# Kernel optimization log

Hardware: AMD Instinct MI355X
Metric: run time of the kernel (lower is better)

The kernel has to match this reference:

```python
import jax, jax.numpy as jnp
import numpy as np

NUM_HEADS = 16
D_MODEL = 1024
NEG_INF = -1e30


def setup_inputs() -> dict:
    key = jax.random.key(0)
    ks = jax.random.split(key, 7)
    B, S, D = 2, 2048, D_MODEL
    scale = 1.0 / np.sqrt(D)
    return {
        "queries": jax.random.normal(ks[0], (B, S, D), dtype=jnp.float32),
        "keys": jax.random.normal(ks[1], (B, S, D), dtype=jnp.float32),
        "values": jax.random.normal(ks[2], (B, S, D), dtype=jnp.float32),
        "Wq": jax.random.normal(ks[3], (D, D), dtype=jnp.float32) * scale,
        "Wk": jax.random.normal(ks[4], (D, D), dtype=jnp.float32) * scale,
        "Wv": jax.random.normal(ks[5], (D, D), dtype=jnp.float32) * scale,
        "Wo": jax.random.normal(ks[6], (D, D), dtype=jnp.float32) * scale,
    }


def _split_heads(x, h):
    # [B, S, D] -> [B, h, S, D/h]
    B, S, D = x.shape
    return x.reshape(B, S, h, D // h).transpose(0, 2, 1, 3)


def reference(queries, keys, values, Wq, Wk, Wv, Wo):
    h = NUM_HEADS
    q = _split_heads(queries @ Wq, h)  # [B, h, S, dh]
    k = _split_heads(keys @ Wk, h)
    v = _split_heads(values @ Wv, h)
    dh = q.shape[-1]
    scores = jnp.einsum("bhqd,bhkd->bhqk", q, k) / jnp.sqrt(jnp.float32(dh))
    # original quirk: exactly-zero scores are masked to -1e30 before softmax
    scores = jnp.where(scores == 0, NEG_INF, scores)
    attn = jax.nn.softmax(scores, axis=-1)
    out = jnp.einsum("bhqk,bhkd->bhqd", attn, v)  # [B, h, S, dh]
    B, _, S, _ = out.shape
    out = out.transpose(0, 2, 1, 3).reshape(B, S, h * dh)
    return out @ Wo
```

## Files before the change

kernel.cpp:

```cpp
#include <hip/hip_runtime.h>

typedef unsigned short u16;
typedef short bf16x8 __attribute__((ext_vector_type(8)));
typedef float f32x4 __attribute__((ext_vector_type(4)));
typedef float f32x16 __attribute__((ext_vector_type(16)));

namespace {

constexpr int kB = 2, kS = 2048, kD = 1024, kH = 16, kDh = 64;
constexpr float kC2 = 0.125f * 1.44269504088896341f;

__device__ inline u16 f32_bf16(float f) {
    unsigned u = __float_as_uint(f);
    u += 0x7FFFu + ((u >> 16) & 1u);
    return (u16)(u >> 16);
}

__device__ inline u16 f32_bf16_fast(float f) {
    return (u16)((__float_as_uint(f) + 0x8000u) >> 16);
}

__device__ inline float fast_exp2(float x) {
    float r;
    asm("v_exp_f32 %0, %1" : "=v"(r) : "v"(x));
    return r;
}

__device__ inline void gl_lds16(const void* g, void* l) {
    __builtin_amdgcn_global_load_lds(
        (const __attribute__((address_space(1))) void*)g,
        (__attribute__((address_space(3))) void*)l, 16, 0, 0);
}

__device__ inline int swz8(int l) {
    return ((l & 3) ^ ((l >> 2) & 3) ^ ((l >> 4) & 3)) * 8;
}

__global__ __launch_bounds__(256) void prep(
    const float* __restrict__ s0, const float* __restrict__ s1,
    const float* __restrict__ s2,
    u16* __restrict__ d0, u16* __restrict__ d1, u16* __restrict__ d2,
    const float* __restrict__ W0, const float* __restrict__ W1,
    const float* __restrict__ W2, const float* __restrict__ W3,
    u16* __restrict__ T0, u16* __restrict__ T1,
    u16* __restrict__ T2, u16* __restrict__ T3)
{
    const int y = blockIdx.y;
    if (y < 3) {
        const float* src = y == 0 ? s0 : (y == 1 ? s1 : s2);
        u16* dst = y == 0 ? d0 : (y == 1 ? d1 : d2);
        const int i = blockIdx.x * 256 + threadIdx.x;
        const float4* s4 = (const float4*)src;
        float4 a = s4[2 * i], b = s4[2 * i + 1];
        uint4 o;
        o.x = (unsigned)f32_bf16(a.x) | ((unsigned)f32_bf16(a.y) << 16);
        o.y = (unsigned)f32_bf16(a.z) | ((unsigned)f32_bf16(a.w) << 16);
        o.z = (unsigned)f32_bf16(b.x) | ((unsigned)f32_bf16(b.y) << 16);
        o.w = (unsigned)f32_bf16(b.z) | ((unsigned)f32_bf16(b.w) << 16);
        ((uint4*)dst)[i] = o;
        return;
    }
    if (blockIdx.x >= 256) return;
    const int z = y - 3;
    const float* W = z == 0 ? W0 : (z == 1 ? W1 : (z == 2 ? W2 : W3));
    u16* Wt = z == 0 ? T0 : (z == 1 ? T1 : (z == 2 ? T2 : T3));
    const float sc = (z == 0) ? kC2 : 1.0f;

    __shared__ __attribute__((aligned(16))) u16 T[64][65];
    const int t = threadIdx.x;
    const int n0 = (blockIdx.x & 15) * 64, k0 = (blockIdx.x >> 4) * 64;
    const int r = t >> 4, c4 = (t & 15) * 4;
#pragma unroll
    for (int it = 0; it < 4; ++it) {
        const int rr = r + 16 * it;
        float4 v = *(const float4*)(W + (size_t)(k0 + rr) * kD + n0 + c4);
        T[rr][c4 + 0] = f32_bf16(v.x * sc);
        T[rr][c4 + 1] = f32_bf16(v.y * sc);
        T[rr][c4 + 2] = f32_bf16(v.z * sc);
        T[rr][c4 + 3] = f32_bf16(v.w * sc);
    }
    __syncthreads();
#pragma unroll
    for (int it = 0; it < 4; ++it) {
        const int nn = r + 16 * it;
        uint2 pk;
        pk.x = (unsigned)T[c4 + 0][nn] | ((unsigned)T[c4 + 1][nn] << 16);
        pk.y = (unsigned)T[c4 + 2][nn] | ((unsigned)T[c4 + 3][nn] << 16);
        *(uint2*)(Wt + (size_t)(n0 + nn) * kD + k0 + c4) = pk;
    }
}

__global__ __launch_bounds__(256) void vtrans(
    const u16* __restrict__ V, u16* __restrict__ Vt)
{
    __shared__ __attribute__((aligned(16))) u16 T[64][65];
    const int t = threadIdx.x;
    const int s0 = blockIdx.x * 64;
    const int bh = blockIdx.y, b = bh >> 4, h = bh & 15;
    const int rr = t >> 3, c0 = (t & 7) * 8;
    union { u16 u[8]; uint4 v4; } buf;
#pragma unroll
    for (int p = 0; p < 2; ++p) {
        const int s = rr + 32 * p;
        buf.v4 = *(const uint4*)(V + (size_t)(b * kS + s0 + s) * kD + h * kDh + c0);
#pragma unroll
        for (int i = 0; i < 8; ++i) T[c0 + i][s] = buf.u[i];
    }
    __syncthreads();
#pragma unroll
    for (int p = 0; p < 2; ++p) {
        const int d = rr + 32 * p;
#pragma unroll
        for (int i = 0; i < 8; ++i) buf.u[i] = T[d][c0 + i];
        *(uint4*)(Vt + (size_t)(bh * kDh + d) * kS + s0 + c0) = buf.v4;
    }
}

template <bool F32OUT>
__device__ inline void gemm128_body(
    const u16* __restrict__ A, const u16* __restrict__ Wt,
    void* __restrict__ Cout, int M, int N, int K, int bx, int by)
{
    __shared__ __attribute__((aligned(16))) u16 As[128 * 32];
    __shared__ __attribute__((aligned(16))) u16 Bs[128 * 32];
    const int t = threadIdx.x, w = t >> 6, l = t & 63;
    const int quad = l >> 4, c = l & 15;
    const int wm = w >> 1, wn = w & 1;
    const int m0 = by * 128, n0 = bx * 128;
    const int lr = l >> 2, lc = swz8(l);
    const int xc = ((quad ^ (c & 3) ^ ((c >> 2) & 3))) * 8;

    const u16* ga0 = A  + (size_t)(m0 + w * 32 + lr) * K + lc;
    const u16* ga1 = A  + (size_t)(m0 + w * 32 + 16 + lr) * K + lc;
    const u16* gb0 = Wt + (size_t)(n0 + w * 32 + lr) * K + lc;
    const u16* gb1 = Wt + (size_t)(n0 + w * 32 + 16 + lr) * K + lc;
    u16* la0 = &As[(w * 32) * 32];
    u16* la1 = &As[(w * 32 + 16) * 32];
    u16* lb0 = &Bs[(w * 32) * 32];
    u16* lb1 = &Bs[(w * 32 + 16) * 32];

    f32x4 acc[4][4];
#pragma unroll
    for (int mi = 0; mi < 4; ++mi)
#pragma unroll
        for (int nj = 0; nj < 4; ++nj) acc[mi][nj] = 0;

    for (int k0 = 0; k0 < K; k0 += 32) {
        gl_lds16(ga0 + k0, la0);
        gl_lds16(ga1 + k0, la1);
        gl_lds16(gb0 + k0, lb0);
        gl_lds16(gb1 + k0, lb1);
        __syncthreads();
        bf16x8 af[4], bf[4];
#pragma unroll
        for (int mi = 0; mi < 4; ++mi)
            af[mi] = *(const bf16x8*)&As[(wm * 64 + mi * 16 + c) * 32 + xc];
#pragma unroll
        for (int nj = 0; nj < 4; ++nj)
            bf[nj] = *(const bf16x8*)&Bs[(wn * 64 + nj * 16 + c) * 32 + xc];
#pragma unroll
        for (int mi = 0; mi < 4; ++mi)
#pragma unroll
            for (int nj = 0; nj < 4; ++nj)
                acc[mi][nj] = __builtin_amdgcn_mfma_f32_16x16x32_bf16(
                    af[mi], bf[nj], acc[mi][nj], 0, 0, 0);
        __syncthreads();
    }

#pragma unroll
    for (int mi = 0; mi < 4; ++mi)
#pragma unroll
        for (int nj = 0; nj < 4; ++nj)
#pragma unroll
            for (int r = 0; r < 4; ++r) {
                const size_t row = m0 + wm * 64 + mi * 16 + quad * 4 + r;
                const size_t col = n0 + wn * 64 + nj * 16 + c;
                if (F32OUT)
                    ((float*)Cout)[row * N + col] = acc[mi][nj][r];
                else
                    ((u16*)Cout)[row * N + col] = f32_bf16(acc[mi][nj][r]);
            }
}

__global__ __launch_bounds__(256) void gemm_qkv(
    const u16* __restrict__ A0, const u16* __restrict__ A1,
    const u16* __restrict__ A2,
    const u16* __restrict__ W0, const u16* __restrict__ W1,
    const u16* __restrict__ W2,
    u16* __restrict__ C0, u16* __restrict__ C1, u16* __restrict__ C2)
{
    const int z = blockIdx.z;
    const u16* A  = z == 0 ? A0 : (z == 1 ? A1 : A2);
    const u16* Wt = z == 0 ? W0 : (z == 1 ? W1 : W2);
    u16* C = z == 0 ? C0 : (z == 1 ? C1 : C2);
    gemm128_body<false>(A, Wt, C, kB * kS, kD, kD, blockIdx.x, blockIdx.y);
}

__global__ __launch_bounds__(256) void gemm_out(
    const u16* __restrict__ A, const u16* __restrict__ Wt,
    float* __restrict__ C)
{
    __shared__ __attribute__((aligned(16))) u16 As[64 * 32];
    __shared__ __attribute__((aligned(16))) u16 Bs[128 * 32];
    const int N = kD, K = kD;
    const int t = threadIdx.x, w = t >> 6, l = t & 63;
    const int quad = l >> 4, c = l & 15;
    const int wm = w >> 1, wn = w & 1;
    const int m0 = blockIdx.y * 64, n0 = blockIdx.x * 128;
    const int lr = l >> 2, lc = swz8(l);
    const int xc = ((quad ^ (c & 3) ^ ((c >> 2) & 3))) * 8;

    const u16* ga  = A  + (size_t)(m0 + w * 16 + lr) * K + lc;
    const u16* gb0 = Wt + (size_t)(n0 + w * 16 + lr) * K + lc;
    const u16* gb1 = Wt + (size_t)(n0 + 64 + w * 16 + lr) * K + lc;
    u16* la  = &As[(w * 16) * 32];
    u16* lb0 = &Bs[(w * 16) * 32];
    u16* lb1 = &Bs[(64 + w * 16) * 32];

    f32x4 acc[2][4];
#pragma unroll
    for (int mi = 0; mi < 2; ++mi)
#pragma unroll
        for (int nj = 0; nj < 4; ++nj) acc[mi][nj] = 0;

    for (int k0 = 0; k0 < K; k0 += 32) {
        gl_lds16(ga + k0, la);
        gl_lds16(gb0 + k0, lb0);
        gl_lds16(gb1 + k0, lb1);
        __syncthreads();
        bf16x8 af[2], bf[4];
#pragma unroll
        for (int mi = 0; mi < 2; ++mi)
            af[mi] = *(const bf16x8*)&As[(wm * 32 + mi * 16 + c) * 32 + xc];
#pragma unroll
        for (int nj = 0; nj < 4; ++nj)
            bf[nj] = *(const bf16x8*)&Bs[(wn * 64 + nj * 16 + c) * 32 + xc];
#pragma unroll
        for (int mi = 0; mi < 2; ++mi)
#pragma unroll
            for (int nj = 0; nj < 4; ++nj)
                acc[mi][nj] = __builtin_amdgcn_mfma_f32_16x16x32_bf16(
                    af[mi], bf[nj], acc[mi][nj], 0, 0, 0);
        __syncthreads();
    }

#pragma unroll
    for (int mi = 0; mi < 2; ++mi)
#pragma unroll
        for (int nj = 0; nj < 4; ++nj)
#pragma unroll
            for (int r = 0; r < 4; ++r) {
                const size_t row = m0 + wm * 32 + mi * 16 + quad * 4 + r;
                const size_t col = n0 + wn * 64 + nj * 16 + c;
                C[row * N + col] = acc[mi][nj][r];
            }
}

__global__ __launch_bounds__(256) void attn(
    const u16* __restrict__ Q, const u16* __restrict__ K,
    const u16* __restrict__ Vt, u16* __restrict__ AO)
{
    __shared__ __attribute__((aligned(16))) u16 KsA[64 * 64];
    __shared__ __attribute__((aligned(16))) u16 KsB[64 * 64];
    __shared__ __attribute__((aligned(16))) u16 VtA[64 * 64];
    __shared__ __attribute__((aligned(16))) u16 VtB[64 * 64];
    __shared__ __attribute__((aligned(16))) u16 Qs[4 * 32 * 64];
    __shared__ __attribute__((aligned(16))) u16 Ps[4 * 32 * 64];

    const int t = threadIdx.x, w = t >> 6, l = t & 63;
    const int half = l >> 5, m = l & 31;
    const int q0 = blockIdx.x * 128;
    const int bh = blockIdx.y, b = bh >> 4, h = bh & 15;
    const int sl = l >> 3;
    const int sc = (l & 7) ^ sl;

    const size_t kbase = (size_t)(b * kS) * kD + h * kDh;
    const size_t vbase = (size_t)bh * kDh * kS;
    const size_t qbase = (size_t)(b * kS + q0 + w * 32) * kD + h * kDh;

    auto stage = [&](int kt, u16* KsP, u16* VtP) {
#pragma unroll
        for (int i = 0; i < 2; ++i) {
            const int R0 = w * 16 + i * 8;
            gl_lds16(K + kbase + (size_t)(kt * 64 + R0 + sl) * kD + sc * 8,
                     &KsP[R0 * 64]);
            gl_lds16(Vt + vbase + (size_t)(R0 + sl) * kS + kt * 64 + sc * 8,
                     &VtP[R0 * 64]);
        }
    };

#pragma unroll
    for (int i = 0; i < 4; ++i)
        gl_lds16(Q + qbase + (size_t)(i * 8 + sl) * kD + sc * 8,
                 &Qs[w * 2048 + i * 512]);
    stage(0, KsA, VtA);
    __syncthreads();

    bf16x8 qf[4];
#pragma unroll
    for (int ch = 0; ch < 4; ++ch)
        qf[ch] = *(const bf16x8*)
            &Qs[w * 2048 + m * 64 + ((2 * ch + half) ^ (m & 7)) * 8];

    bf16x8 ones;
#pragma unroll
    for (int i = 0; i < 8; ++i) ones[i] = (short)0x3F80;

    f32x16 o0 = 0, o1 = 0, ol = 0;

    auto compute = [&](const u16* KsP, const u16* VtP) {
        f32x16 s0 = 0, s1 = 0;
#pragma unroll
        for (int ch = 0; ch < 4; ++ch) {
            const int xo = ((2 * ch + half) ^ (m & 7)) * 8;
            const bf16x8 kf0 = *(const bf16x8*)&KsP[(m) * 64 + xo];
            const bf16x8 kf1 = *(const bf16x8*)&KsP[(32 + m) * 64 + xo];
            s0 = __builtin_amdgcn_mfma_f32_32x32x16_bf16(qf[ch], kf0, s0, 0, 0, 0);
            s1 = __builtin_amdgcn_mfma_f32_32x32x16_bf16(qf[ch], kf1, s1, 0, 0, 0);
        }
#pragma unroll
        for (int reg = 0; reg < 16; ++reg) {
            const int qrow = (reg & 3) + 8 * (reg >> 2) + 4 * half;
            const int base = w * 2048 + qrow * 64;
            const int sw = (qrow & 7);
            {
                const int key = m;
                Ps[base + ((key >> 3) ^ sw) * 8 + (key & 7)] =
                    f32_bf16_fast(fast_exp2(s0[reg]));
            }
            {
                const int key = 32 + m;
                Ps[base + ((key >> 3) ^ sw) * 8 + (key & 7)] =
                    f32_bf16_fast(fast_exp2(s1[reg]));
            }
        }
#pragma unroll
        for (int ch = 0; ch < 4; ++ch) {
            const int xo = ((2 * ch + half) ^ (m & 7)) * 8;
            const bf16x8 pf = *(const bf16x8*)&Ps[w * 2048 + m * 64 + xo];
            const bf16x8 vf0 = *(const bf16x8*)&VtP[(m) * 64 + xo];
            const bf16x8 vf1 = *(const bf16x8*)&VtP[(32 + m) * 64 + xo];
            o0 = __builtin_amdgcn_mfma_f32_32x32x16_bf16(pf, vf0, o0, 0, 0, 0);
            o1 = __builtin_amdgcn_mfma_f32_32x32x16_bf16(pf, vf1, o1, 0, 0, 0);
            ol = __builtin_amdgcn_mfma_f32_32x32x16_bf16(pf, ones, ol, 0, 0, 0);
        }
    };

    constexpr int NT = kS / 64;
#pragma unroll 1
    for (int kt = 0; kt < NT; kt += 2) {
        if (kt + 1 < NT) stage(kt + 1, KsB, VtB);
        compute(KsA, VtA);
        __syncthreads();
        if (kt + 2 < NT) stage(kt + 2, KsA, VtA);
        compute(KsB, VtB);
        __syncthreads();
    }

    const size_t obase = (size_t)(b * kS + q0 + w * 32) * kD + h * kDh;
#pragma unroll
    for (int reg = 0; reg < 16; ++reg) {
        const int qrow = (reg & 3) + 8 * (reg >> 2) + 4 * half;
        const float inv = 1.0f / ol[reg];
        AO[obase + (size_t)qrow * kD + m]      = f32_bf16(o0[reg] * inv);
        AO[obase + (size_t)qrow * kD + 32 + m] = f32_bf16(o1[reg] * inv);
    }
}

}

extern "C" void kernel_launch(void* const* d_in, const int* in_sizes, int n_in,
                              void* d_out, int out_size, void* d_ws, size_t ws_size,
                              hipStream_t stream)
{
    const float* q_in = (const float*)d_in[0];
    const float* k_in = (const float*)d_in[1];
    const float* v_in = (const float*)d_in[2];
    const float* Wq   = (const float*)d_in[3];
    const float* Wk   = (const float*)d_in[4];
    const float* Wv   = (const float*)d_in[5];
    const float* Wo   = (const float*)d_in[6];

    u16* ws = (u16*)d_ws;
    const size_t M1 = 1u << 20;
    u16* xq  = ws;
    u16* xk  = ws + 4 * M1;
    u16* xv  = ws + 8 * M1;
    u16* Wtq = ws + 12 * M1;
    u16* Wtk = ws + 13 * M1;
    u16* Wtv = ws + 14 * M1;
    u16* Wto = ws + 15 * M1;
    u16* Qp  = ws + 16 * M1;
    u16* Kp  = ws + 20 * M1;
    u16* Vp  = ws + 24 * M1;
    u16* AO  = ws + 28 * M1;
    u16* Vtg = xq;

    hipLaunchKernelGGL(prep, dim3(2048, 7), dim3(256), 0, stream,
                       q_in, k_in, v_in, xq, xk, xv,
                       Wq, Wk, Wv, Wo, Wtq, Wtk, Wtv, Wto);

    hipLaunchKernelGGL(gemm_qkv, dim3(8, 32, 3), dim3(256), 0, stream,
                       xq, xk, xv, Wtq, Wtk, Wtv, Qp, Kp, Vp);

    hipLaunchKernelGGL(vtrans, dim3(32, 32), dim3(256), 0, stream, Vp, Vtg);

    hipLaunchKernelGGL(attn, dim3(16, 32), dim3(256), 0, stream, Qp, Kp, Vtg, AO);

    hipLaunchKernelGGL(gemm_out, dim3(8, 64), dim3(256), 0, stream,
                       AO, Wto, (float*)d_out);
}
```

Before: 224.6 us.

## Keep attention P in registers via transposed MFMA and permlane swap

Computes S transposed (K times Q) so the exp'd scores can be packed with v_cvt_pk_bf16_f32 and rearranged by v_permlane32_swap to feed the PV MFMA directly, removing the Ps LDS round trip and the Qs staging. It replaces the extra ones-MFMA row-sum with a VALU accumulation plus a cross-half shuffle, adds s_setprio around MFMA phases, and writes the output through LDS for coalesced 16-byte stores. The added risks are subtle lane-layout mismatches and reuse of K/V LDS buffers for the epilogue after the final barrier.

```diff
diff --git a/kernel.cpp b/kernel.cpp
--- a/kernel.cpp
+++ b/kernel.cpp
@@ -16,14 +16,20 @@
     return (u16)(u >> 16);
 }
 
-__device__ inline u16 f32_bf16_fast(float f) {
-    return (u16)((__float_as_uint(f) + 0x8000u) >> 16);
-}
-
 __device__ inline float fast_exp2(float x) {
     float r;
     asm("v_exp_f32 %0, %1" : "=v"(r) : "v"(x));
     return r;
+}
+
+__device__ inline unsigned cvtpk(float a, float b) {
+    unsigned r;
+    asm("v_cvt_pk_bf16_f32 %0, %1, %2" : "=v"(r) : "v"(a), "v"(b));
+    return r;
+}
+
+__device__ inline void plswap(unsigned& a, unsigned& b) {
+    asm("v_permlane32_swap_b32 %0, %1" : "+v"(a), "+v"(b));
 }
 
 __device__ inline void gl_lds16(const void* g, void* l) {
@@ -264,86 +270,93 @@
     __shared__ __attribute__((aligned(16))) u16 KsB[64 * 64];
     __shared__ __attribute__((aligned(16))) u16 VtA[64 * 64];
     __shared__ __attribute__((aligned(16))) u16 VtB[64 * 64];
-    __shared__ __attribute__((aligned(16))) u16 Qs[4 * 32 * 64];
-    __shared__ __attribute__((aligned(16))) u16 Ps[4 * 32 * 64];
 
     const int t = threadIdx.x, w = t >> 6, l = t & 63;
     const int half = l >> 5, m = l & 31;
     const int q0 = blockIdx.x * 128;
     const int bh = blockIdx.y, b = bh >> 4, h = bh & 15;
-    const int sl = l >> 3;
-    const int sc = (l & 7) ^ sl;
+    const int sr = l >> 3;
+    const int sc = (l & 7) ^ sr;
 
     const size_t kbase = (size_t)(b * kS) * kD + h * kDh;
     const size_t vbase = (size_t)bh * kDh * kS;
-    const size_t qbase = (size_t)(b * kS + q0 + w * 32) * kD + h * kDh;
 
     auto stage = [&](int kt, u16* KsP, u16* VtP) {
 #pragma unroll
         for (int i = 0; i < 2; ++i) {
             const int R0 = w * 16 + i * 8;
-            gl_lds16(K + kbase + (size_t)(kt * 64 + R0 + sl) * kD + sc * 8,
+            gl_lds16(K + kbase + (size_t)(kt * 64 + R0 + sr) * kD + sc * 8,
                      &KsP[R0 * 64]);
-            gl_lds16(Vt + vbase + (size_t)(R0 + sl) * kS + kt * 64 + sc * 8,
+            gl_lds16(Vt + vbase + (size_t)(R0 + sr) * kS + kt * 64 + sc * 8,
                      &VtP[R0 * 64]);
         }
     };
 
-#pragma unroll
-    for (int i = 0; i < 4; ++i)
-        gl_lds16(Q + qbase + (size_t)(i * 8 + sl) * kD + sc * 8,
-                 &Qs[w * 2048 + i * 512]);
     stage(0, KsA, VtA);
+
+    bf16x8 qf[4];
+    {
+        const u16* qp = Q + (size_t)(b * kS + q0 + w * 32 + m) * kD
+                        + h * kDh + half * 8;
+#pragma unroll
+        for (int ch = 0; ch < 4; ++ch)
+            qf[ch] = *(const bf16x8*)(qp + ch * 16);
+    }
+
+    f32x16 o0 = 0, o1 = 0;
+    f32x4 lsum = 0;
+
     __syncthreads();
-
-    bf16x8 qf[4];
-#pragma unroll
-    for (int ch = 0; ch < 4; ++ch)
-        qf[ch] = *(const bf16x8*)
-            &Qs[w * 2048 + m * 64 + ((2 * ch + half) ^ (m & 7)) * 8];
-
-    bf16x8 ones;
-#pragma unroll
-    for (int i = 0; i < 8; ++i) ones[i] = (short)0x3F80;
-
-    f32x16 o0 = 0, o1 = 0, ol = 0;
 
     auto compute = [&](const u16* KsP, const u16* VtP) {
         f32x16 s0 = 0, s1 = 0;
+        __builtin_amdgcn_s_setprio(1);
 #pragma unroll
         for (int ch = 0; ch < 4; ++ch) {
             const int xo = ((2 * ch + half) ^ (m & 7)) * 8;
             const bf16x8 kf0 = *(const bf16x8*)&KsP[(m) * 64 + xo];
             const bf16x8 kf1 = *(const bf16x8*)&KsP[(32 + m) * 64 + xo];
-            s0 = __builtin_amdgcn_mfma_f32_32x32x16_bf16(qf[ch], kf0, s0, 0, 0, 0);
-            s1 = __builtin_amdgcn_mfma_f32_32x32x16_bf16(qf[ch], kf1, s1, 0, 0, 0);
+            s0 = __builtin_amdgcn_mfma_f32_32x32x16_bf16(kf0, qf[ch], s0, 0, 0, 0);
+            s1 = __builtin_amdgcn_mfma_f32_32x32x16_bf16(kf1, qf[ch], s1, 0, 0, 0);
         }
-#pragma unroll
-        for (int reg = 0; reg < 16; ++reg) {
-            const int qrow = (reg & 3) + 8 * (reg >> 2) + 4 * half;
-            const int base = w * 2048 + qrow * 64;
-            const int sw = (qrow & 7);
-            {
-                const int key = m;
-                Ps[base + ((key >> 3) ^ sw) * 8 + (key & 7)] =
-                    f32_bf16_fast(fast_exp2(s0[reg]));
+        __builtin_amdgcn_s_setprio(0);
+#pragma unroll
+        for (int r = 0; r < 16; ++r) {
+            s0[r] = fast_exp2(s0[r]);
+            s1[r] = fast_exp2(s1[r]);
+        }
+#pragma unroll
+        for (int r = 0; r < 16; r += 4) {
+            lsum += (f32x4){s0[r], s0[r + 1], s0[r + 2], s0[r + 3]};
+            lsum += (f32x4){s1[r], s1[r + 1], s1[r + 2], s1[r + 3]};
+        }
+        __builtin_amdgcn_s_setprio(1);
+#pragma unroll
+        for (int ts = 0; ts < 4; ++ts) {
+            const int rb = (ts & 1) * 8;
+            unsigned c0, c1, c2, c3;
+            if (ts < 2) {
+                c0 = cvtpk(s0[rb + 0], s0[rb + 1]);
+                c1 = cvtpk(s0[rb + 2], s0[rb + 3]);
+                c2 = cvtpk(s0[rb + 4], s0[rb + 5]);
+                c3 = cvtpk(s0[rb + 6], s0[rb + 7]);
+            } else {
+                c0 = cvtpk(s1[rb + 0], s1[rb + 1]);
+                c1 = cvtpk(s1[rb + 2], s1[rb + 3]);
+                c2 = cvtpk(s1[rb + 4], s1[rb + 5]);
+                c3 = cvtpk(s1[rb + 6], s1[rb + 7]);
             }
-            {
-                const int key = 32 + m;
-                Ps[base + ((key >> 3) ^ sw) * 8 + (key & 7)] =
-                    f32_bf16_fast(fast_exp2(s1[reg]));
-            }
-        }
-#pragma unroll
-        for (int ch = 0; ch < 4; ++ch) {
-            const int xo = ((2 * ch + half) ^ (m & 7)) * 8;
-            const bf16x8 pf = *(const bf16x8*)&Ps[w * 2048 + m * 64 + xo];
+            plswap(c0, c2);
+            plswap(c1, c3);
+            union { unsigned u[4]; bf16x8 v; } pb;
+            pb.u[0] = c0; pb.u[1] = c1; pb.u[2] = c2; pb.u[3] = c3;
+            const int xo = ((2 * ts + half) ^ (m & 7)) * 8;
             const bf16x8 vf0 = *(const bf16x8*)&VtP[(m) * 64 + xo];
             const bf16x8 vf1 = *(const bf16x8*)&VtP[(32 + m) * 64 + xo];
-            o0 = __builtin_amdgcn_mfma_f32_32x32x16_bf16(pf, vf0, o0, 0, 0, 0);
-            o1 = __builtin_amdgcn_mfma_f32_32x32x16_bf16(pf, vf1, o1, 0, 0, 0);
-            ol = __builtin_amdgcn_mfma_f32_32x32x16_bf16(pf, ones, ol, 0, 0, 0);
+            o0 = __builtin_amdgcn_mfma_f32_32x32x16_bf16(vf0, pb.v, o0, 0, 0, 0);
+            o1 = __builtin_amdgcn_mfma_f32_32x32x16_bf16(vf1, pb.v, o1, 0, 0, 0);
         }
+        __builtin_amdgcn_s_setprio(0);
     };
 
     constexpr int NT = kS / 64;
@@ -357,13 +370,28 @@
         __syncthreads();
     }
 
+    float lt = lsum[0] + lsum[1] + lsum[2] + lsum[3];
+    lt += __shfl_xor(lt, 32, 64);
+    const float inv = 1.0f / lt;
+
+    u16* ob = w == 0 ? KsA : (w == 1 ? KsB : (w == 2 ? VtA : VtB));
+#pragma unroll
+    for (int r = 0; r < 4; ++r) {
+        uint2 p0, p1;
+        p0.x = cvtpk(o0[4 * r + 0] * inv, o0[4 * r + 1] * inv);
+        p0.y = cvtpk(o0[4 * r + 2] * inv, o0[4 * r + 3] * inv);
+        p1.x = cvtpk(o1[4 * r + 0] * inv, o1[4 * r + 1] * inv);
+        p1.y = cvtpk(o1[4 * r + 2] * inv, o1[4 * r + 3] * inv);
+        *(uint2*)&ob[m * 64 + ((r ^ (m & 7)) << 3) + 4 * half] = p0;
+        *(uint2*)&ob[m * 64 + (((4 + r) ^ (m & 7)) << 3) + 4 * half] = p1;
+    }
     const size_t obase = (size_t)(b * kS + q0 + w * 32) * kD + h * kDh;
 #pragma unroll
-    for (int reg = 0; reg < 16; ++reg) {
-        const int qrow = (reg & 3) + 8 * (reg >> 2) + 4 * half;
-        const float inv = 1.0f / ol[reg];
-        AO[obase + (size_t)qrow * kD + m]      = f32_bf16(o0[reg] * inv);
-        AO[obase + (size_t)qrow * kD + 32 + m] = f32_bf16(o1[reg] * inv);
+    for (int i = 0; i < 4; ++i) {
+        const int q = l >> 1;
+        const int tt = (l & 1) + i * 2;
+        uint4 dd = *(const uint4*)&ob[q * 64 + ((tt ^ (q & 7)) << 3)];
+        *(uint4*)(AO + obase + (size_t)q * kD + tt * 8) = dd;
     }
 }
 
```

Result: faster. 216.7 us (-3.5%).
